# Kernel optimization log

Measured on AMD Instinct MI355X. Metric: run time of the kernel, lower is better.

Reference implementation:

```python
import jax, jax.numpy as jnp
import numpy as np
import math

B, S, D = 2, 2048, 2048
N_HEADS, N_KV = 32, 8
HD = D // N_HEADS  # 64
N_REP = N_HEADS // N_KV  # 4


def setup_inputs() -> dict:
    key = jax.random.key(0)
    ks = jax.random.split(key, 6)
    x = jax.random.normal(ks[0], (B, S, D), dtype=jnp.float32)
    # rotary frequencies: freqs_cis[t, j] = exp(i * t * theta^{-2j/hd})
    theta = 10000.0
    inv_freq = 1.0 / (theta ** (np.arange(0, HD, 2, dtype=np.float32) / HD))  # [HD/2]
    t = np.arange(S, dtype=np.float32)
    ang = np.outer(t, inv_freq)  # [S, HD/2]
    freqs_cos = jnp.asarray(np.cos(ang), dtype=jnp.float32)
    freqs_sin = jnp.asarray(np.sin(ang), dtype=jnp.float32)
    # causal additive mask (0 on/below diagonal, -inf above)
    mask = jnp.where(jnp.tril(jnp.ones((S, S), dtype=bool)), 0.0, -jnp.inf).astype(jnp.float32)
    scale = 0.02
    wq = jax.random.normal(ks[1], (D, N_HEADS * HD), dtype=jnp.float32) * scale
    wk = jax.random.normal(ks[2], (D, N_KV * HD), dtype=jnp.float32) * scale
    wv = jax.random.normal(ks[3], (D, N_KV * HD), dtype=jnp.float32) * scale
    wo = jax.random.normal(ks[4], (N_HEADS * HD, D), dtype=jnp.float32) * scale
    return {"x": x, "freqs_cos": freqs_cos, "freqs_sin": freqs_sin, "mask": mask,
            "wq": wq, "wk": wk, "wv": wv, "wo": wo, "start_pos": 0}


def _rope(t, cos, sin):
    # t: [b, s, h, hd]; cos/sin: [s, hd/2]; complex multiply on (even, odd) pairs
    tr = t.reshape(*t.shape[:-1], HD // 2, 2)
    a, b = tr[..., 0], tr[..., 1]
    c = cos[None, :, None, :]
    s = sin[None, :, None, :]
    out = jnp.stack([a * c - b * s, a * s + b * c], axis=-1)
    return out.reshape(t.shape)


def reference(x, freqs_cos, freqs_sin, mask, wq, wk, wv, wo, start_pos):
    b, s, _ = x.shape
    q = jnp.einsum('bsd,de->bse', x, wq).reshape(b, s, N_HEADS, HD)
    k = jnp.einsum('bsd,de->bse', x, wk).reshape(b, s, N_KV, HD)
    v = jnp.einsum('bsd,de->bse', x, wv).reshape(b, s, N_KV, HD)
    q = _rope(q, freqs_cos[:s], freqs_sin[:s])
    k = _rope(k, freqs_cos[:s], freqs_sin[:s])
    # GQA: query head h = kv_head * n_rep + r  (matches repeat_kv layout)
    qg = q.reshape(b, s, N_KV, N_REP, HD)
    scores = jnp.einsum('bqgrd,bkgd->bgrqk', qg, k) / math.sqrt(HD)
    scores = scores + mask[None, None, None, :s, :s]
    probs = jax.nn.softmax(scores, axis=-1)
    out = jnp.einsum('bgrqk,bkgd->bqgrd', probs, v)  # [b, s, n_kv, n_rep, hd]
    out = out.reshape(b, s, N_HEADS * HD)
    return jnp.einsum('bse,ed->bsd', out, wo)
```

## Files before the change

kernel.cpp:

```cpp
#include <hip/hip_runtime.h>
#include <hip/hip_bf16.h>

typedef unsigned short u16;
typedef __bf16 bf16x8 __attribute__((ext_vector_type(8)));
typedef float f32x4 __attribute__((ext_vector_type(4)));
typedef u16 u16x4 __attribute__((ext_vector_type(4)));

__device__ __forceinline__ u16 f2bf(float f) {
    __bf16 h = (__bf16)f;
    return __builtin_bit_cast(u16, h);
}
__device__ __forceinline__ float bf2f(u16 u) {
    __bf16 h = __builtin_bit_cast(__bf16, u);
    return (float)h;
}

#define MFMA16(a, b, c) __builtin_amdgcn_mfma_f32_16x16x32_bf16(a, b, c, 0, 0, 0)

__device__ __forceinline__ void gload_lds16(const u16* g, u16* l) {
    __builtin_amdgcn_global_load_lds((const __attribute__((address_space(1))) void*)g,
                                     (__attribute__((address_space(3))) void*)l, 16, 0, 0);
}

__global__ __launch_bounds__(256) void cast_bf16(const float* __restrict__ in,
                                                 u16* __restrict__ out, int n4) {
    int i = blockIdx.x * 256 + threadIdx.x;
    if (i >= n4) return;
    float4 a = ((const float4*)in)[i];
    u16x4 u;
    u[0] = f2bf(a.x); u[1] = f2bf(a.y); u[2] = f2bf(a.z); u[3] = f2bf(a.w);
    ((u16x4*)out)[i] = u;
}

__global__ __launch_bounds__(256) void transpose_cast(const float* __restrict__ in,
                                                      u16* __restrict__ out, int R, int C) {
    __shared__ u16 tile[64][65];
    const int tc = blockIdx.x * 64, tr = blockIdx.y * 64;
    const int lr = threadIdx.x >> 6, lc = threadIdx.x & 63;
#pragma unroll
    for (int i = 0; i < 16; i++) {
        int r = i * 4 + lr;
        tile[r][lc] = f2bf(in[(size_t)(tr + r) * C + tc + lc]);
    }
    __syncthreads();
#pragma unroll
    for (int i = 0; i < 16; i++) {
        int r = i * 4 + lr;
        out[(size_t)(tc + r) * R + tr + lc] = tile[lc][r];
    }
}

template <int F32OUT>
__global__ __launch_bounds__(256) void gemm_bt(const u16* __restrict__ A,
                                               const u16* __restrict__ Bt,
                                               void* __restrict__ C, int M, int N, int K) {
    __shared__ u16 As[128 * 32];
    __shared__ u16 Bs[128 * 32];
    const int tid = threadIdx.x;
    const int wave = tid >> 6, lane = tid & 63;
    const int l15 = lane & 15, l16 = lane >> 4;
    const int row0 = blockIdx.y * 128, col0 = blockIdx.x * 128;
    const int wr = (wave >> 1) * 64, wc = (wave & 1) * 64;
    const int c0 = wave * 128 + lane;
    const int c1 = c0 + 64;
    const int rA0 = c0 >> 2, ccA0 = (c0 & 3) * 8;
    const int rA1 = c1 >> 2, ccA1 = (c1 & 3) * 8;
    const u16* Ab = A + (size_t)row0 * K;
    const u16* Bb = Bt + (size_t)col0 * K;

    f32x4 acc[4][4] = {};

    for (int kt = 0; kt < K; kt += 32) {
        __syncthreads();
        gload_lds16(Ab + (size_t)rA0 * K + kt + ccA0, &As[(wave * 2 + 0) * 512]);
        gload_lds16(Ab + (size_t)rA1 * K + kt + ccA1, &As[(wave * 2 + 1) * 512]);
        gload_lds16(Bb + (size_t)rA0 * K + kt + ccA0, &Bs[(wave * 2 + 0) * 512]);
        gload_lds16(Bb + (size_t)rA1 * K + kt + ccA1, &Bs[(wave * 2 + 1) * 512]);
        __syncthreads();
        bf16x8 af[4], bfr[4];
#pragma unroll
        for (int m = 0; m < 4; m++)
            af[m] = *(const bf16x8*)&As[(wr + m * 16 + l15) * 32 + l16 * 8];
#pragma unroll
        for (int n = 0; n < 4; n++)
            bfr[n] = *(const bf16x8*)&Bs[(wc + n * 16 + l15) * 32 + l16 * 8];
#pragma unroll
        for (int m = 0; m < 4; m++)
#pragma unroll
            for (int n = 0; n < 4; n++)
                acc[m][n] = MFMA16(af[m], bfr[n], acc[m][n]);
    }

#pragma unroll
    for (int m = 0; m < 4; m++)
#pragma unroll
        for (int n = 0; n < 4; n++)
#pragma unroll
            for (int r = 0; r < 4; r++) {
                size_t ci = (size_t)(row0 + wr + m * 16 + l16 * 4 + r) * N +
                            (col0 + wc + n * 16 + l15);
                if (F32OUT)
                    ((float*)C)[ci] = acc[m][n][r];
                else
                    ((u16*)C)[ci] = f2bf(acc[m][n][r]);
            }
}

__global__ __launch_bounds__(256) void rope_q(u16* __restrict__ q,
                                              const float* __restrict__ fc,
                                              const float* __restrict__ fs) {
    int idx = blockIdx.x * 256 + threadIdx.x;
    int i = idx & 31;
    int s = (idx >> 10) & 2047;
    unsigned int v = ((unsigned int*)q)[idx];
    float a = bf2f((u16)(v & 0xffff)), b = bf2f((u16)(v >> 16));
    float c = fc[s * 32 + i], sn = fs[s * 32 + i];
    unsigned int o = (unsigned int)f2bf(a * c - b * sn) |
                     ((unsigned int)f2bf(a * sn + b * c) << 16);
    ((unsigned int*)q)[idx] = o;
}

__global__ __launch_bounds__(256) void rope_k_pack(const u16* __restrict__ kv,
                                                   const float* __restrict__ fc,
                                                   const float* __restrict__ fs,
                                                   u16* __restrict__ kb) {
    int idx = blockIdx.x * 256 + threadIdx.x;
    int i = idx & 31;
    int g = (idx >> 5) & 7;
    int s = (idx >> 8) & 2047;
    int b = idx >> 19;
    unsigned int v = ((const unsigned int*)kv)[(size_t)(b * 2048 + s) * 512 + g * 32 + i];
    float a = bf2f((u16)(v & 0xffff)), bb = bf2f((u16)(v >> 16));
    float c = fc[s * 32 + i], sn = fs[s * 32 + i];
    unsigned int o = (unsigned int)f2bf(a * c - bb * sn) |
                     ((unsigned int)f2bf(a * sn + bb * c) << 16);
    ((unsigned int*)kb)[(size_t)((b * 8 + g) * 2048 + s) * 32 + i] = o;
}

__global__ __launch_bounds__(256) void v_transpose(const u16* __restrict__ kv,
                                                   u16* __restrict__ vt) {
    __shared__ u16 tile[64][65];
    const int st = blockIdx.x, g = blockIdx.y, b = blockIdx.z;
    const int lr = threadIdx.x >> 6, lc = threadIdx.x & 63;
#pragma unroll
    for (int i = 0; i < 16; i++) {
        int s = st * 64 + i * 4 + lr;
        tile[i * 4 + lr][lc] = kv[(size_t)(b * 2048 + s) * 1024 + 512 + g * 64 + lc];
    }
    __syncthreads();
#pragma unroll
    for (int i = 0; i < 16; i++) {
        int d = i * 4 + lr;
        vt[(size_t)((b * 8 + g) * 64 + d) * 2048 + st * 64 + lc] = tile[lc][d];
    }
}

__global__ __launch_bounds__(512) void flash(const u16* __restrict__ Q,
                                             const u16* __restrict__ Kb,
                                             const u16* __restrict__ Vt,
                                             u16* __restrict__ O) {
    __shared__ u16 Ks[2][4096];
    __shared__ u16 Vs[2][4096];
    __shared__ u16 Pl[8][2048];
    const int b = blockIdx.z, h = blockIdx.y;
    const int qt = blockIdx.z ? blockIdx.x : 7 - blockIdx.x;
    const int g = h >> 2;
    const int wave = threadIdx.x >> 6, lane = threadIdx.x & 63;
    const int l15 = lane & 15, l16 = lane >> 4;
    const int sw = l15 & 7;
    const int q0 = qt * 256 + wave * 32;
    const int KT = qt * 4 + 4;

    const u16* Kg = Kb + (size_t)(b * 8 + g) * 2048 * 64;
    const u16* Vg = Vt + (size_t)(b * 8 + g) * 64 * 2048;

    const int rloc = lane >> 3;
    const int jg = (lane & 7) ^ rloc;
    const u16* gK = Kg + (size_t)(wave * 8 + rloc) * 64 + jg * 8;
    const u16* gV = Vg + (size_t)(wave * 8 + rloc) * 2048 + jg * 8;

    bf16x8 qf[2][2];
#pragma unroll
    for (int m = 0; m < 2; m++) {
        const u16* qp = Q + (size_t)(b * 2048 + q0 + m * 16 + l15) * 2048 + h * 64 + l16 * 8;
#pragma unroll
        for (int cc = 0; cc < 2; cc++) {
            bf16x8 v = *(const bf16x8*)(qp + cc * 32);
#pragma unroll
            for (int j = 0; j < 8; j++) v[j] = (__bf16)((float)v[j] * 0.125f);
            qf[m][cc] = v;
        }
    }

    f32x4 o[2][4] = {};
    float mr[2][4], ls[2][4];
#pragma unroll
    for (int m = 0; m < 2; m++)
#pragma unroll
        for (int r = 0; r < 4; r++) { mr[m][r] = -1e30f; ls[m][r] = 0.f; }
    u16* Pw = Pl[wave];

    gload_lds16(gK, &Ks[0][wave * 512]);
    gload_lds16(gV, &Vs[0][wave * 512]);
    __syncthreads();

    for (int kt = 0; kt < KT; kt++) {
        const int cur = kt & 1;
        if (kt + 1 < KT) {
            gload_lds16(gK + (size_t)(kt + 1) * 4096, &Ks[cur ^ 1][wave * 512]);
            gload_lds16(gV + (kt + 1) * 64, &Vs[cur ^ 1][wave * 512]);
        }
        if (kt * 64 <= q0 + 31) {
            f32x4 s[2][4];
#pragma unroll
            for (int m = 0; m < 2; m++)
#pragma unroll
                for (int sub = 0; sub < 4; sub++) s[m][sub] = (f32x4){0.f, 0.f, 0.f, 0.f};
#pragma unroll
            for (int sub = 0; sub < 4; sub++) {
                const int krow = sub * 16 + l15;
#pragma unroll
                for (int cc = 0; cc < 2; cc++) {
                    bf16x8 kf =
                        *(const bf16x8*)&Ks[cur][krow * 64 + (((cc * 4 + l16) ^ sw) * 8)];
                    s[0][sub] = MFMA16(qf[0][cc], kf, s[0][sub]);
                    s[1][sub] = MFMA16(qf[1][cc], kf, s[1][sub]);
                }
            }
            if (kt * 64 + 63 > q0) {
#pragma unroll
                for (int sub = 0; sub < 4; sub++)
#pragma unroll
                    for (int m = 0; m < 2; m++)
#pragma unroll
                        for (int r = 0; r < 4; r++) {
                            int kcol = kt * 64 + sub * 16 + l15;
                            int qrow = q0 + m * 16 + l16 * 4 + r;
                            if (kcol > qrow) s[m][sub][r] = -1e30f;
                        }
            }
            float mx[2][4];
#pragma unroll
            for (int m = 0; m < 2; m++)
#pragma unroll
                for (int r = 0; r < 4; r++)
                    mx[m][r] = fmaxf(fmaxf(s[m][0][r], s[m][1][r]),
                                     fmaxf(s[m][2][r], s[m][3][r]));
#pragma unroll
            for (int d = 1; d < 16; d <<= 1)
#pragma unroll
                for (int m = 0; m < 2; m++)
#pragma unroll
                    for (int r = 0; r < 4; r++)
                        mx[m][r] = fmaxf(mx[m][r], __shfl_xor(mx[m][r], d));
            float al[2][4];
#pragma unroll
            for (int m = 0; m < 2; m++)
#pragma unroll
                for (int r = 0; r < 4; r++) {
                    float mn = fmaxf(mr[m][r], mx[m][r]);
                    al[m][r] = __expf(mr[m][r] - mn);
                    mr[m][r] = mn;
                }
            float rs[2][4] = {};
#pragma unroll
            for (int sub = 0; sub < 4; sub++)
#pragma unroll
                for (int m = 0; m < 2; m++)
#pragma unroll
                    for (int r = 0; r < 4; r++) {
                        float p = __expf(s[m][sub][r] - mr[m][r]);
                        s[m][sub][r] = p;
                        rs[m][r] += p;
                    }
#pragma unroll
            for (int d = 1; d < 16; d <<= 1)
#pragma unroll
                for (int m = 0; m < 2; m++)
#pragma unroll
                    for (int r = 0; r < 4; r++) rs[m][r] += __shfl_xor(rs[m][r], d);
#pragma unroll
            for (int m = 0; m < 2; m++)
#pragma unroll
                for (int r = 0; r < 4; r++) ls[m][r] = ls[m][r] * al[m][r] + rs[m][r];
#pragma unroll
            for (int m = 0; m < 2; m++)
#pragma unroll
                for (int n = 0; n < 4; n++)
#pragma unroll
                    for (int r = 0; r < 4; r++) o[m][n][r] *= al[m][r];
#pragma unroll
            for (int sub = 0; sub < 4; sub++)
#pragma unroll
                for (int m = 0; m < 2; m++)
#pragma unroll
                    for (int r = 0; r < 4; r++) {
                        int row = m * 16 + l16 * 4 + r, col = sub * 16 + l15;
                        Pw[row * 64 + (((col >> 3) ^ (row & 7)) * 8) + (col & 7)] =
                            f2bf(s[m][sub][r]);
                    }
#pragma unroll
            for (int cc = 0; cc < 2; cc++) {
                bf16x8 pa0 = *(const bf16x8*)&Pw[l15 * 64 + (((cc * 4 + l16) ^ sw) * 8)];
                bf16x8 pa1 =
                    *(const bf16x8*)&Pw[(16 + l15) * 64 + (((cc * 4 + l16) ^ sw) * 8)];
#pragma unroll
                for (int n = 0; n < 4; n++) {
                    const int vrow = n * 16 + l15;
                    bf16x8 vf =
                        *(const bf16x8*)&Vs[cur][vrow * 64 + (((cc * 4 + l16) ^ sw) * 8)];
                    o[0][n] = MFMA16(pa0, vf, o[0][n]);
                    o[1][n] = MFMA16(pa1, vf, o[1][n]);
                }
            }
        }
        __syncthreads();
    }
#pragma unroll
    for (int m = 0; m < 2; m++)
#pragma unroll
        for (int r = 0; r < 4; r++) {
            float inv = 1.f / ls[m][r];
#pragma unroll
            for (int n = 0; n < 4; n++) {
                size_t oi = (size_t)(b * 2048 + q0 + m * 16 + l16 * 4 + r) * 2048 + h * 64 +
                            n * 16 + l15;
                O[oi] = f2bf(o[m][n][r] * inv);
            }
        }
}

extern "C" void kernel_launch(void* const* d_in, const int* in_sizes, int n_in,
                              void* d_out, int out_size, void* d_ws, size_t ws_size,
                              hipStream_t stream) {
    const float* x = (const float*)d_in[0];
    const float* fc = (const float*)d_in[1];
    const float* fs = (const float*)d_in[2];
    const float* wq = (const float*)d_in[4];
    const float* wk = (const float*)d_in[5];
    const float* wv = (const float*)d_in[6];
    const float* wo = (const float*)d_in[7];
    float* out = (float*)d_out;

    u16* ws = (u16*)d_ws;
    u16* xb = ws;
    u16* wq_t = xb + (size_t)4096 * 2048;
    u16* wkv_t = wq_t + (size_t)2048 * 2048;
    u16* wo_t = wkv_t + (size_t)1024 * 2048;
    u16* qb = wo_t + (size_t)2048 * 2048;
    u16* kvb = qb + (size_t)4096 * 2048;
    u16* kb = kvb + (size_t)4096 * 1024;
    u16* vt = kb + (size_t)2 * 8 * 2048 * 64;
    u16* ab = xb;

    cast_bf16<<<8192, 256, 0, stream>>>(x, xb, 4096 * 2048 / 4);
    transpose_cast<<<dim3(32, 32), 256, 0, stream>>>(wq, wq_t, 2048, 2048);
    transpose_cast<<<dim3(8, 32), 256, 0, stream>>>(wk, wkv_t, 2048, 512);
    transpose_cast<<<dim3(8, 32), 256, 0, stream>>>(wv, wkv_t + (size_t)512 * 2048, 2048, 512);
    transpose_cast<<<dim3(32, 32), 256, 0, stream>>>(wo, wo_t, 2048, 2048);

    gemm_bt<0><<<dim3(16, 32), 256, 0, stream>>>(xb, wq_t, qb, 4096, 2048, 2048);
    gemm_bt<0><<<dim3(8, 32), 256, 0, stream>>>(xb, wkv_t, kvb, 4096, 1024, 2048);

    rope_q<<<16384, 256, 0, stream>>>(qb, fc, fs);
    rope_k_pack<<<4096, 256, 0, stream>>>(kvb, fc, fs, kb);
    v_transpose<<<dim3(32, 8, 2), 256, 0, stream>>>(kvb, vt);

    flash<<<dim3(8, 32, 2), 512, 0, stream>>>(qb, kb, vt, ab);

    gemm_bt<1><<<dim3(16, 32), 256, 0, stream>>>(ab, wo_t, out, 4096, 2048, 2048);
}
```

Measured before the change: 425.4 us.

## Fuse QKV projection GEMM, batch weight transposes, merge rope kernels, add MFMA priority

Concatenates the Q, K and V weights into one transposed matrix so a single 4096x3072 GEMM produces a combined qkv buffer. The four weight transpose launches are merged into one z-indexed kernel, and rope for Q and K is merged into one kernel. Flash and v_transpose now read the strided qkv layout. s_setprio hints are placed around the MFMA blocks in flash. The aim is fewer launches and better GEMM occupancy, at the cost of a wider row stride for the Q reads.

```diff
diff --git a/kernel.cpp b/kernel.cpp
--- a/kernel.cpp
+++ b/kernel.cpp
@@ -32,8 +32,22 @@
     ((u16x4*)out)[i] = u;
 }
 
-__global__ __launch_bounds__(256) void transpose_cast(const float* __restrict__ in,
-                                                      u16* __restrict__ out, int R, int C) {
+__global__ __launch_bounds__(256) void transpose_all(const float* __restrict__ wq,
+                                                     const float* __restrict__ wk,
+                                                     const float* __restrict__ wv,
+                                                     const float* __restrict__ wo,
+                                                     u16* __restrict__ wqkv_t,
+                                                     u16* __restrict__ wo_t) {
+    const int z = blockIdx.z;
+    const float* in;
+    u16* out;
+    int C;
+    if (z == 0)      { in = wq; out = wqkv_t;                     C = 2048; }
+    else if (z == 1) { in = wk; out = wqkv_t + (size_t)2048 * 2048; C = 512; }
+    else if (z == 2) { in = wv; out = wqkv_t + (size_t)2560 * 2048; C = 512; }
+    else             { in = wo; out = wo_t;                       C = 2048; }
+    if (blockIdx.x * 64 >= C) return;
+
     __shared__ u16 tile[64][65];
     const int tc = blockIdx.x * 64, tr = blockIdx.y * 64;
     const int lr = threadIdx.x >> 6, lc = threadIdx.x & 63;
@@ -46,7 +60,7 @@
 #pragma unroll
     for (int i = 0; i < 16; i++) {
         int r = i * 4 + lr;
-        out[(size_t)(tc + r) * R + tr + lc] = tile[lc][r];
+        out[(size_t)(tc + r) * 2048 + tr + lc] = tile[lc][r];
     }
 }
 
@@ -106,38 +120,40 @@
             }
 }
 
-__global__ __launch_bounds__(256) void rope_q(u16* __restrict__ q,
-                                              const float* __restrict__ fc,
-                                              const float* __restrict__ fs) {
+__global__ __launch_bounds__(256) void rope_qk(u16* __restrict__ qkv,
+                                               const float* __restrict__ fc,
+                                               const float* __restrict__ fs,
+                                               u16* __restrict__ kb) {
     int idx = blockIdx.x * 256 + threadIdx.x;
-    int i = idx & 31;
-    int s = (idx >> 10) & 2047;
-    unsigned int v = ((unsigned int*)q)[idx];
-    float a = bf2f((u16)(v & 0xffff)), b = bf2f((u16)(v >> 16));
-    float c = fc[s * 32 + i], sn = fs[s * 32 + i];
-    unsigned int o = (unsigned int)f2bf(a * c - b * sn) |
-                     ((unsigned int)f2bf(a * sn + b * c) << 16);
-    ((unsigned int*)q)[idx] = o;
-}
-
-__global__ __launch_bounds__(256) void rope_k_pack(const u16* __restrict__ kv,
-                                                   const float* __restrict__ fc,
-                                                   const float* __restrict__ fs,
-                                                   u16* __restrict__ kb) {
-    int idx = blockIdx.x * 256 + threadIdx.x;
-    int i = idx & 31;
-    int g = (idx >> 5) & 7;
-    int s = (idx >> 8) & 2047;
-    int b = idx >> 19;
-    unsigned int v = ((const unsigned int*)kv)[(size_t)(b * 2048 + s) * 512 + g * 32 + i];
-    float a = bf2f((u16)(v & 0xffff)), bb = bf2f((u16)(v >> 16));
-    float c = fc[s * 32 + i], sn = fs[s * 32 + i];
-    unsigned int o = (unsigned int)f2bf(a * c - bb * sn) |
-                     ((unsigned int)f2bf(a * sn + bb * c) << 16);
-    ((unsigned int*)kb)[(size_t)((b * 8 + g) * 2048 + s) * 32 + i] = o;
-}
-
-__global__ __launch_bounds__(256) void v_transpose(const u16* __restrict__ kv,
+    unsigned int* q32 = (unsigned int*)qkv;
+    if (idx < 2 * 2048 * 32 * 32) {
+        int i = idx & 31;
+        int h = (idx >> 5) & 31;
+        int s = (idx >> 10) & 2047;
+        int b = idx >> 21;
+        size_t a = (size_t)(b * 2048 + s) * 1536 + h * 32 + i;
+        unsigned int v = q32[a];
+        float x = bf2f((u16)(v & 0xffff)), y = bf2f((u16)(v >> 16));
+        float c = fc[s * 32 + i], sn = fs[s * 32 + i];
+        q32[a] = (unsigned int)f2bf(x * c - y * sn) |
+                 ((unsigned int)f2bf(x * sn + y * c) << 16);
+    } else {
+        int j = idx - 2 * 2048 * 32 * 32;
+        int i = j & 31;
+        int g = (j >> 5) & 7;
+        int s = (j >> 8) & 2047;
+        int b = j >> 19;
+        size_t a = (size_t)(b * 2048 + s) * 1536 + 1024 + g * 32 + i;
+        unsigned int v = q32[a];
+        float x = bf2f((u16)(v & 0xffff)), y = bf2f((u16)(v >> 16));
+        float c = fc[s * 32 + i], sn = fs[s * 32 + i];
+        ((unsigned int*)kb)[(size_t)((b * 8 + g) * 2048 + s) * 32 + i] =
+            (unsigned int)f2bf(x * c - y * sn) |
+            ((unsigned int)f2bf(x * sn + y * c) << 16);
+    }
+}
+
+__global__ __launch_bounds__(256) void v_transpose(const u16* __restrict__ qkv,
                                                    u16* __restrict__ vt) {
     __shared__ u16 tile[64][65];
     const int st = blockIdx.x, g = blockIdx.y, b = blockIdx.z;
@@ -145,7 +161,7 @@
 #pragma unroll
     for (int i = 0; i < 16; i++) {
         int s = st * 64 + i * 4 + lr;
-        tile[i * 4 + lr][lc] = kv[(size_t)(b * 2048 + s) * 1024 + 512 + g * 64 + lc];
+        tile[i * 4 + lr][lc] = qkv[(size_t)(b * 2048 + s) * 3072 + 2560 + g * 64 + lc];
     }
     __syncthreads();
 #pragma unroll
@@ -182,7 +198,7 @@
     bf16x8 qf[2][2];
 #pragma unroll
     for (int m = 0; m < 2; m++) {
-        const u16* qp = Q + (size_t)(b * 2048 + q0 + m * 16 + l15) * 2048 + h * 64 + l16 * 8;
+        const u16* qp = Q + (size_t)(b * 2048 + q0 + m * 16 + l15) * 3072 + h * 64 + l16 * 8;
 #pragma unroll
         for (int cc = 0; cc < 2; cc++) {
             bf16x8 v = *(const bf16x8*)(qp + cc * 32);
@@ -216,6 +232,7 @@
             for (int m = 0; m < 2; m++)
 #pragma unroll
                 for (int sub = 0; sub < 4; sub++) s[m][sub] = (f32x4){0.f, 0.f, 0.f, 0.f};
+            __builtin_amdgcn_s_setprio(1);
 #pragma unroll
             for (int sub = 0; sub < 4; sub++) {
                 const int krow = sub * 16 + l15;
@@ -227,6 +244,7 @@
                     s[1][sub] = MFMA16(qf[1][cc], kf, s[1][sub]);
                 }
             }
+            __builtin_amdgcn_s_setprio(0);
             if (kt * 64 + 63 > q0) {
 #pragma unroll
                 for (int sub = 0; sub < 4; sub++)
@@ -299,6 +317,7 @@
                         Pw[row * 64 + (((col >> 3) ^ (row & 7)) * 8) + (col & 7)] =
                             f2bf(s[m][sub][r]);
                     }
+            __builtin_amdgcn_s_setprio(1);
 #pragma unroll
             for (int cc = 0; cc < 2; cc++) {
                 bf16x8 pa0 = *(const bf16x8*)&Pw[l15 * 64 + (((cc * 4 + l16) ^ sw) * 8)];
@@ -313,6 +332,7 @@
                     o[1][n] = MFMA16(pa1, vf, o[1][n]);
                 }
             }
+            __builtin_amdgcn_s_setprio(0);
         }
         __syncthreads();
     }
@@ -344,29 +364,22 @@
 
     u16* ws = (u16*)d_ws;
     u16* xb = ws;
-    u16* wq_t = xb + (size_t)4096 * 2048;
-    u16* wkv_t = wq_t + (size_t)2048 * 2048;
-    u16* wo_t = wkv_t + (size_t)1024 * 2048;
-    u16* qb = wo_t + (size_t)2048 * 2048;
-    u16* kvb = qb + (size_t)4096 * 2048;
-    u16* kb = kvb + (size_t)4096 * 1024;
+    u16* wqkv_t = xb + (size_t)4096 * 2048;
+    u16* wo_t = wqkv_t + (size_t)3072 * 2048;
+    u16* qkv = wo_t + (size_t)2048 * 2048;
+    u16* kb = qkv + (size_t)4096 * 3072;
     u16* vt = kb + (size_t)2 * 8 * 2048 * 64;
     u16* ab = xb;
 
     cast_bf16<<<8192, 256, 0, stream>>>(x, xb, 4096 * 2048 / 4);
-    transpose_cast<<<dim3(32, 32), 256, 0, stream>>>(wq, wq_t, 2048, 2048);
-    transpose_cast<<<dim3(8, 32), 256, 0, stream>>>(wk, wkv_t, 2048, 512);
-    transpose_cast<<<dim3(8, 32), 256, 0, stream>>>(wv, wkv_t + (size_t)512 * 2048, 2048, 512);
-    transpose_cast<<<dim3(32, 32), 256, 0, stream>>>(wo, wo_t, 2048, 2048);
-
-    gemm_bt<0><<<dim3(16, 32), 256, 0, stream>>>(xb, wq_t, qb, 4096, 2048, 2048);
-    gemm_bt<0><<<dim3(8, 32), 256, 0, stream>>>(xb, wkv_t, kvb, 4096, 1024, 2048);
-
-    rope_q<<<16384, 256, 0, stream>>>(qb, fc, fs);
-    rope_k_pack<<<4096, 256, 0, stream>>>(kvb, fc, fs, kb);
-    v_transpose<<<dim3(32, 8, 2), 256, 0, stream>>>(kvb, vt);
-
-    flash<<<dim3(8, 32, 2), 512, 0, stream>>>(qb, kb, vt, ab);
+    transpose_all<<<dim3(32, 32, 4), 256, 0, stream>>>(wq, wk, wv, wo, wqkv_t, wo_t);
+
+    gemm_bt<0><<<dim3(24, 32), 256, 0, stream>>>(xb, wqkv_t, qkv, 4096, 3072, 2048);
+
+    rope_qk<<<20480, 256, 0, stream>>>(qkv, fc, fs, kb);
+    v_transpose<<<dim3(32, 8, 2), 256, 0, stream>>>(qkv, vt);
+
+    flash<<<dim3(8, 32, 2), 512, 0, stream>>>(qkv, kb, vt, ab);
 
     gemm_bt<1><<<dim3(16, 32), 256, 0, stream>>>(ab, wo_t, out, 4096, 2048, 2048);
 }
```

New measurement: 394.3 us. 7.3% less time.
